# Optimization experiments

Measured on AMD Instinct MI355X. Metric: run time of the kernel, lower is better.

## Reference

```python
import jax, jax.numpy as jnp
import numpy as np

N, C, H, W = 4, 256, 128, 128
BLOCK = 8
FWB = H // BLOCK  # feature_size_with_block = 16
N_BBOX = 100
M = N_BBOX * N * FWB * FWB  # 102400 rois


def setup_inputs() -> dict:
    key = jax.random.key(0)
    ks = jax.random.split(key, 6)
    s = 1.0 / np.sqrt(C).astype(np.float32)
    return {
        "feature": jax.random.normal(ks[0], (N, C, H, W), jnp.float32),
        "rois_feature": jax.random.normal(ks[1], (M, C, 1, 1), jnp.float32),
        "W_weight": jax.random.normal(ks[2], (C, C), jnp.float32) * s,
        "b_weight": jnp.zeros((C,), jnp.float32),
        "W_fuse": jax.random.normal(ks[3], (C, C), jnp.float32) * s,
        "b_fuse": jnp.zeros((C,), jnp.float32),
        "W_pw": jax.random.normal(ks[4], (BLOCK * BLOCK, C), jnp.float32) * s,
        "b_pw": jnp.zeros((BLOCK * BLOCK,), jnp.float32),
        "feature_size_with_block": FWB,
    }


def reference(feature, rois_feature, W_weight, b_weight, W_fuse, b_fuse, W_pw, b_pw, feature_size_with_block):
    n, c, h, w = feature.shape
    f = feature_size_with_block
    blk = h // f  # block_size
    m = rois_feature.shape[0]
    n_bbox = m // (n * f * f)

    x = rois_feature[:, :, 0, 0]  # [M, C] (1x1 conv on 1x1 spatial == dense layer)
    feat_w = jax.nn.relu(x @ W_weight.T + b_weight)  # [M, C]
    feat_f = jax.nn.relu(x @ W_fuse.T + b_fuse)      # [M, C]
    point_weight = feat_w @ W_pw.T + b_pw            # [M, B*B]

    # [n_bbox, N, F, F, B, B] -> [N, n_bbox, F, F, B, B]
    pw = point_weight.reshape(n_bbox, n, f, f, blk, blk).transpose(1, 0, 2, 3, 4, 5)
    # feature -> blocks: [N, C, F, B, F, B] -> [N, C, F, F, B, B]
    fb = feature.reshape(n, c, f, blk, f, blk).transpose(0, 1, 2, 4, 3, 5)
    # weighted block-sum without materializing the n_bbox-repeated tensor.
    # torch: sum over (B,B) -> [N,nb,C,F,F], then permute(1,0,3,4,2) -> [nb,N,F,F,C]
    out = jnp.einsum('ncpqab,nkpqab->knpqc', fb, pw)  # [nb, N, F, F, C]
    out = out.reshape(m, c)[:, :, None, None]          # [M, C, 1, 1]
    fused = feat_f[:, :, None, None] + out
    return fused, out
```

## Files before the change

### kernel.cpp

```cpp
#include <hip/hip_runtime.h>

#define NN 4
#define CC 256
#define HH 128
#define FWBv 16
#define BLK 8
#define NBBOX 100
#define MM (NBBOX * NN * FWBv * FWBv)

typedef __attribute__((ext_vector_type(8))) short bf16x8;
typedef __attribute__((ext_vector_type(4))) float f32x4;

__device__ __forceinline__ unsigned short f2bf(float x) {
  union { float f; unsigned int u; } v; v.f = x;
  unsigned int r = v.u + 0x7FFFu + ((v.u >> 16) & 1u);
  return (unsigned short)(r >> 16);
}

__device__ __forceinline__ float bfbits2f(unsigned int hi16) {
  union { float f; unsigned int u; } v; v.u = hi16;
  return v.f;
}

__device__ __forceinline__ void async16(const void* g, void* l) {
  __builtin_amdgcn_global_load_lds(
      (__attribute__((address_space(1))) void*)(g),
      (__attribute__((address_space(3))) void*)(l), 16, 0, 0);
}

__global__ __launch_bounds__(256) void k_convert(
    const float* __restrict__ Wf, const float* __restrict__ Ww,
    const float* __restrict__ Wpw,
    unsigned short* __restrict__ oWf, unsigned short* __restrict__ oWw,
    unsigned short* __restrict__ oWpw) {
  int i = blockIdx.x * 256 + threadIdx.x;
  oWf[i] = f2bf(Wf[i]);
  oWw[i] = f2bf(Ww[i]);
  if (i < 64 * 256) oWpw[i] = f2bf(Wpw[i]);
}


__device__ __forceinline__ void stage_w(const unsigned short* __restrict__ Wp,
                                        int kc, unsigned short* buf, int w,
                                        int lane) {
  const int srcs = ((lane & 3) ^ ((lane >> 3) & 3)) * 8;
  const int rr = lane >> 2;
#pragma unroll
  for (int i = 0; i < 4; ++i) {
    const int r0 = w * 64 + i * 16;
    async16(Wp + (size_t)(r0 + rr) * 256 + kc * 32 + srcs, buf + r0 * 32);
  }
}

__device__ __forceinline__ void stage_wpw(const unsigned short* __restrict__ Wpw,
                                          unsigned short* buf, int kc4, int w,
                                          int lane) {
  const int srcs = ((lane & 7) ^ ((lane >> 3) & 7)) * 8;
  const int rr = lane >> 3;
#pragma unroll
  for (int i = 0; i < 2; ++i) {
    const int r0 = w * 16 + i * 8;
    async16(Wpw + (size_t)(r0 + rr) * 256 + kc4 * 64 + srcs, buf + r0 * 64);
  }
}

__device__ __forceinline__ void body16(const unsigned short* buf,
                                       const unsigned short (*xsp)[264],
                                       int kcol, int w, int lr, int quad,
                                       int wslot, f32x4 acc[4][4]) {
  bf16x8 aw[4], bx[4];
#pragma unroll
  for (int nt = 0; nt < 4; ++nt)
    aw[nt] = *(const bf16x8*)&buf[(w * 64 + nt * 16 + lr) * 32 + wslot];
#pragma unroll
  for (int mt = 0; mt < 4; ++mt)
    bx[mt] = *(const bf16x8*)&xsp[mt * 16 + lr][kcol];
  __builtin_amdgcn_s_setprio(1);
#pragma unroll
  for (int mt = 0; mt < 4; ++mt)
#pragma unroll
    for (int nt = 0; nt < 4; ++nt)
      acc[mt][nt] = __builtin_amdgcn_mfma_f32_16x16x32_bf16(
          aw[nt], bx[mt], acc[mt][nt], 0, 0, 0);
  __builtin_amdgcn_s_setprio(0);
}

__global__ __launch_bounds__(256) void k1(
    const float* __restrict__ rois,
    const unsigned short* __restrict__ Wf,
    const unsigned short* __restrict__ Ww,
    const unsigned short* __restrict__ Wpw,
    const float* __restrict__ bf_, const float* __restrict__ bw_,
    const float* __restrict__ bpw_,
    float* __restrict__ out_slot)
{
  __shared__ __align__(16) unsigned short xs[64][264];
  __shared__ __align__(16) unsigned short bs[2][8192];
  unsigned short* bsf = &bs[0][0];
  unsigned short* os = (unsigned short*)out_slot;
  const int t = threadIdx.x;
  const int lane = t & 63, w = t >> 6;
  const int lr = lane & 15, quad = lane >> 4;
  const int row_base = blockIdx.x * 64;
  const int wslot = (quad ^ ((lr >> 1) & 3)) << 3;

  stage_w(Wf, 0, &bs[0][0], w, lane);

#pragma unroll
  for (int i = 0; i < 16; ++i) {
    const int elem = (i * 256 + t) * 4;
    const int r = elem >> 8, c = elem & 255;
    const float4 v = *(const float4*)(rois + (size_t)row_base * 256 + elem);
    unsigned int lo = f2bf(v.x) | ((unsigned int)f2bf(v.y) << 16);
    unsigned int hi = f2bf(v.z) | ((unsigned int)f2bf(v.w) << 16);
    *(uint2*)&xs[r][c] = make_uint2(lo, hi);
  }
  asm volatile("s_waitcnt vmcnt(0) lgkmcnt(0)" ::: "memory");
  __builtin_amdgcn_s_barrier();

  f32x4 acc[4][4];
#pragma unroll
  for (int mt = 0; mt < 4; ++mt)
#pragma unroll
    for (int nt = 0; nt < 4; ++nt) acc[mt][nt] = (f32x4){0.f, 0.f, 0.f, 0.f};

#pragma unroll
  for (int kc = 0; kc < 8; ++kc) {
    if (kc < 7) stage_w(Wf, kc + 1, &bs[(kc + 1) & 1][0], w, lane);
    else        stage_w(Ww, 0, &bs[0][0], w, lane);
    asm volatile("s_waitcnt vmcnt(4)" ::: "memory");
    body16(&bs[kc & 1][0], xs, kc * 32 + quad * 8, w, lr, quad, wslot, acc);
  }

#pragma unroll
  for (int nt = 0; nt < 4; ++nt) {
    const int col0 = w * 64 + nt * 16 + quad * 4;
    const float4 b4 = *(const float4*)(bf_ + col0);
#pragma unroll
    for (int mt = 0; mt < 4; ++mt) {
      float v0 = acc[mt][nt][0] + b4.x; v0 = v0 > 0.f ? v0 : 0.f;
      float v1 = acc[mt][nt][1] + b4.y; v1 = v1 > 0.f ? v1 : 0.f;
      float v2 = acc[mt][nt][2] + b4.z; v2 = v2 > 0.f ? v2 : 0.f;
      float v3 = acc[mt][nt][3] + b4.w; v3 = v3 > 0.f ? v3 : 0.f;
      unsigned int lo = f2bf(v0) | ((unsigned int)f2bf(v1) << 16);
      unsigned int hi = f2bf(v2) | ((unsigned int)f2bf(v3) << 16);
      *(uint2*)&os[(size_t)(row_base + mt * 16 + lr) * 512 + 128 + col0] =
          make_uint2(lo, hi);
      acc[mt][nt] = (f32x4){0.f, 0.f, 0.f, 0.f};
    }
  }

#pragma unroll
  for (int kc = 0; kc < 8; ++kc) {
    if (kc < 7) {
      stage_w(Ww, kc + 1, &bs[(kc + 1) & 1][0], w, lane);
      asm volatile("s_waitcnt vmcnt(4)" ::: "memory");
    } else {
      asm volatile("s_waitcnt vmcnt(0)" ::: "memory");
    }
    body16(&bs[kc & 1][0], xs, kc * 32 + quad * 8, w, lr, quad, wslot, acc);
  }

  __builtin_amdgcn_s_barrier();

#pragma unroll
  for (int c = 0; c < 4; ++c) stage_wpw(Wpw, bsf + c * 4096, c, w, lane);

#pragma unroll
  for (int nt = 0; nt < 4; ++nt) {
    const int col0 = w * 64 + nt * 16 + quad * 4;
    const float4 b4 = *(const float4*)(bw_ + col0);
#pragma unroll
    for (int mt = 0; mt < 4; ++mt) {
      float v0 = acc[mt][nt][0] + b4.x; v0 = v0 > 0.f ? v0 : 0.f;
      float v1 = acc[mt][nt][1] + b4.y; v1 = v1 > 0.f ? v1 : 0.f;
      float v2 = acc[mt][nt][2] + b4.z; v2 = v2 > 0.f ? v2 : 0.f;
      float v3 = acc[mt][nt][3] + b4.w; v3 = v3 > 0.f ? v3 : 0.f;
      unsigned int lo = f2bf(v0) | ((unsigned int)f2bf(v1) << 16);
      unsigned int hi = f2bf(v2) | ((unsigned int)f2bf(v3) << 16);
      *(uint2*)&xs[mt * 16 + lr][col0] = make_uint2(lo, hi);
    }
  }
  asm volatile("s_waitcnt vmcnt(0) lgkmcnt(0)" ::: "memory");
  __builtin_amdgcn_s_barrier();

  f32x4 acc2[4];
#pragma unroll
  for (int mt = 0; mt < 4; ++mt) acc2[mt] = (f32x4){0.f, 0.f, 0.f, 0.f};
#pragma unroll
  for (int c = 0; c < 4; ++c) {
#pragma unroll
    for (int kt = 0; kt < 2; ++kt) {
      const int sl = ((kt * 4 + quad) ^ (lr & 7)) << 3;
      const bf16x8 apw =
          *(const bf16x8*)&bsf[c * 4096 + (w * 16 + lr) * 64 + sl];
      const int kcol = c * 64 + kt * 32 + quad * 8;
      __builtin_amdgcn_s_setprio(1);
#pragma unroll
      for (int mt = 0; mt < 4; ++mt) {
        const bf16x8 bx = *(const bf16x8*)&xs[mt * 16 + lr][kcol];
        acc2[mt] =
            __builtin_amdgcn_mfma_f32_16x16x32_bf16(apw, bx, acc2[mt], 0, 0, 0);
      }
      __builtin_amdgcn_s_setprio(0);
    }
  }
  {
    const int j0 = w * 16 + quad * 4;
    const float4 bj = *(const float4*)(bpw_ + j0);
#pragma unroll
    for (int mt = 0; mt < 4; ++mt) {
      float v0 = acc2[mt][0] + bj.x;
      float v1 = acc2[mt][1] + bj.y;
      float v2 = acc2[mt][2] + bj.z;
      float v3 = acc2[mt][3] + bj.w;
      unsigned int lo = f2bf(v0) | ((unsigned int)f2bf(v1) << 16);
      unsigned int hi = f2bf(v2) | ((unsigned int)f2bf(v3) << 16);
      *(uint2*)&os[(size_t)(row_base + mt * 16 + lr) * 512 + j0] =
          make_uint2(lo, hi);
    }
  }
}

__global__ __launch_bounds__(512) void k2(
    const float* __restrict__ feature,
    float* __restrict__ fused_slot,
    float* __restrict__ out_slot)
{
  __shared__ unsigned short fbuf[256][72];
  __shared__ unsigned short pwb[112][72];
  const int t = threadIdx.x;
  const int lane = t & 63, w = t >> 6;
  const int lr = lane & 15, quad = lane >> 4;
  const int bid = blockIdx.x;
  const int n = bid >> 8, p = (bid >> 4) & 15, q = bid & 15;
  const unsigned short* os = (const unsigned short*)out_slot;

  if (t < 432) {
    const int r = 100 + t / 36, cw = t % 36;
    *(unsigned int*)&pwb[r][cw * 2] = 0u;
  }

  for (int pi = t; pi < 2048; pi += 512) {
    const int c = pi >> 3, a = pi & 7;
    const float* fp =
        feature + (((size_t)n * 256 + c) * 128 + p * 8 + a) * 128 + q * 8;
    const float4 v0 = *(const float4*)fp;
    const float4 v1 = *(const float4*)(fp + 4);
    unsigned int u0 = f2bf(v0.x) | ((unsigned int)f2bf(v0.y) << 16);
    unsigned int u1 = f2bf(v0.z) | ((unsigned int)f2bf(v0.w) << 16);
    unsigned int u2 = f2bf(v1.x) | ((unsigned int)f2bf(v1.y) << 16);
    unsigned int u3 = f2bf(v1.z) | ((unsigned int)f2bf(v1.w) << 16);
    *(uint4*)&fbuf[c][a * 8] = make_uint4(u0, u1, u2, u3);
  }

  for (int pi = t; pi < 1600; pi += 512) {
    const int k = pi >> 4, ch = pi & 15;
    const uint2 v = *(const uint2*)&os[(size_t)(bid + k * 1024) * 512 + ch * 4];
    *(uint2*)&pwb[k][ch * 4] = v;
  }
  __syncthreads();

  uint2 ffp[7][2];
#pragma unroll
  for (int kt = 0; kt < 7; ++kt) {
    const int k = kt * 16 + lr;
    if (k < 100) {
      const size_t ro = (size_t)(bid + k * 1024) * 512;
#pragma unroll
      for (int ct = 0; ct < 2; ++ct) {
        const int c0 = w * 32 + ct * 16 + quad * 4;
        ffp[kt][ct] = *(const uint2*)&os[ro + 128 + c0];
      }
    }
  }

  f32x4 acc[7][2];
#pragma unroll
  for (int kt = 0; kt < 7; ++kt)
#pragma unroll
    for (int ct = 0; ct < 2; ++ct) acc[kt][ct] = (f32x4){0.f, 0.f, 0.f, 0.f};
#pragma unroll
  for (int kj = 0; kj < 2; ++kj) {
    const int kk = kj * 32 + quad * 8;
    bf16x8 pa[7], fa[2];
#pragma unroll
    for (int kt = 0; kt < 7; ++kt)
      pa[kt] = *(const bf16x8*)&pwb[kt * 16 + lr][kk];
#pragma unroll
    for (int ct = 0; ct < 2; ++ct)
      fa[ct] = *(const bf16x8*)&fbuf[w * 32 + ct * 16 + lr][kk];
    __builtin_amdgcn_s_setprio(1);
#pragma unroll
    for (int kt = 0; kt < 7; ++kt)
#pragma unroll
      for (int ct = 0; ct < 2; ++ct)
        acc[kt][ct] = __builtin_amdgcn_mfma_f32_16x16x32_bf16(
            fa[ct], pa[kt], acc[kt][ct], 0, 0, 0);
    __builtin_amdgcn_s_setprio(0);
  }

  asm volatile("s_waitcnt vmcnt(0)" ::: "memory");
  __builtin_amdgcn_s_barrier();

#pragma unroll
  for (int kt = 0; kt < 7; ++kt) {
    const int k = kt * 16 + lr;
    if (k < 100) {
      const size_t ro = (size_t)(bid + k * 1024) * 256;
#pragma unroll
      for (int ct = 0; ct < 2; ++ct) {
        const int c0 = w * 32 + ct * 16 + quad * 4;
        float4 v;
        v.x = acc[kt][ct][0];
        v.y = acc[kt][ct][1];
        v.z = acc[kt][ct][2];
        v.w = acc[kt][ct][3];
        *(float4*)(out_slot + ro + c0) = v;
        const uint2 ff = ffp[kt][ct];
        float4 f;
        f.x = v.x + bfbits2f(ff.x << 16);
        f.y = v.y + bfbits2f(ff.x & 0xffff0000u);
        f.z = v.z + bfbits2f(ff.y << 16);
        f.w = v.w + bfbits2f(ff.y & 0xffff0000u);
        *(float4*)(fused_slot + ro + c0) = f;
      }
    }
  }
}

extern "C" void kernel_launch(void* const* d_in, const int* in_sizes, int n_in,
                              void* d_out, int out_size, void* d_ws, size_t ws_size,
                              hipStream_t stream) {
  const float* feature = (const float*)d_in[0];
  const float* rois = (const float*)d_in[1];
  const float* Ww = (const float*)d_in[2];
  const float* bw = (const float*)d_in[3];
  const float* Wf = (const float*)d_in[4];
  const float* bfv = (const float*)d_in[5];
  const float* Wpw = (const float*)d_in[6];
  const float* bpw = (const float*)d_in[7];

  unsigned short* wsWf = (unsigned short*)d_ws;
  unsigned short* wsWw = wsWf + 256 * 256;
  unsigned short* wsWpw = wsWw + 256 * 256;

  float* fused_slot = (float*)d_out;
  float* out_slot = fused_slot + (size_t)MM * 256;

  k_convert<<<256, 256, 0, stream>>>(Wf, Ww, Wpw, wsWf, wsWw, wsWpw);
  k1<<<MM / 64, 256, 0, stream>>>(rois, wsWf, wsWw, wsWpw, bfv, bw, bpw,
                                  out_slot);
  k2<<<NN * FWBv * FWBv, 512, 0, stream>>>(feature, fused_slot, out_slot);
}
```

Before: 455.8 us.

## Pre-swizzle weights into MFMA fragment order and load them directly into registers

The weight conversion kernel now writes bf16 weights in a fragment-major layout that matches the MFMA A-operand, so k1 can load each fragment straight from global memory into registers. This replaces the async global-to-LDS staging buffers, their waitcnts and the swizzled LDS reads. LDS use drops, which allows a launch bound of 3 blocks per CU for more occupancy. The cost is more VGPRs for the double-buffered fragments and more global/L2 traffic, because every block now reads the weights directly rather than through shared staging.

Result: faster. 441.4 us (-3.1%).

```diff
diff --git a/kernel.cpp b/kernel.cpp
--- a/kernel.cpp
+++ b/kernel.cpp
@@ -22,10 +22,8 @@
   return v.f;
 }
 
-__device__ __forceinline__ void async16(const void* g, void* l) {
-  __builtin_amdgcn_global_load_lds(
-      (__attribute__((address_space(1))) void*)(g),
-      (__attribute__((address_space(3))) void*)(l), 16, 0, 0);
+__device__ __forceinline__ unsigned int pk(float a, float b) {
+  return (unsigned int)f2bf(a) | ((unsigned int)f2bf(b) << 16);
 }
 
 __global__ __launch_bounds__(256) void k_convert(
@@ -33,45 +31,44 @@
     const float* __restrict__ Wpw,
     unsigned short* __restrict__ oWf, unsigned short* __restrict__ oWw,
     unsigned short* __restrict__ oWpw) {
-  int i = blockIdx.x * 256 + threadIdx.x;
-  oWf[i] = f2bf(Wf[i]);
-  oWw[i] = f2bf(Ww[i]);
-  if (i < 64 * 256) oWpw[i] = f2bf(Wpw[i]);
-}
-
-
-__device__ __forceinline__ void stage_w(const unsigned short* __restrict__ Wp,
-                                        int kc, unsigned short* buf, int w,
-                                        int lane) {
-  const int srcs = ((lane & 3) ^ ((lane >> 3) & 3)) * 8;
-  const int rr = lane >> 2;
-#pragma unroll
-  for (int i = 0; i < 4; ++i) {
-    const int r0 = w * 64 + i * 16;
-    async16(Wp + (size_t)(r0 + rr) * 256 + kc * 32 + srcs, buf + r0 * 32);
-  }
-}
-
-__device__ __forceinline__ void stage_wpw(const unsigned short* __restrict__ Wpw,
-                                          unsigned short* buf, int kc4, int w,
-                                          int lane) {
-  const int srcs = ((lane & 7) ^ ((lane >> 3) & 7)) * 8;
-  const int rr = lane >> 3;
-#pragma unroll
-  for (int i = 0; i < 2; ++i) {
-    const int r0 = w * 16 + i * 8;
-    async16(Wpw + (size_t)(r0 + rr) * 256 + kc4 * 64 + srcs, buf + r0 * 64);
-  }
-}
-
-__device__ __forceinline__ void body16(const unsigned short* buf,
-                                       const unsigned short (*xsp)[264],
-                                       int kcol, int w, int lr, int quad,
-                                       int wslot, f32x4 acc[4][4]) {
-  bf16x8 aw[4], bx[4];
-#pragma unroll
-  for (int nt = 0; nt < 4; ++nt)
-    aw[nt] = *(const bf16x8*)&buf[(w * 64 + nt * 16 + lr) * 32 + wslot];
+  const int i = blockIdx.x * 256 + threadIdx.x;
+  if (i < 8192) {
+    const int lane = i & 63, g = (i >> 6) & 15, kc = i >> 10;
+    const int row = g * 16 + (lane & 15);
+    const int col0 = kc * 32 + (lane >> 4) * 8;
+    {
+      const float* s = Wf + (size_t)row * 256 + col0;
+      const float4 a = *(const float4*)s, b = *(const float4*)(s + 4);
+      *(uint4*)(oWf + (size_t)i * 8) =
+          make_uint4(pk(a.x, a.y), pk(a.z, a.w), pk(b.x, b.y), pk(b.z, b.w));
+    }
+    {
+      const float* s = Ww + (size_t)row * 256 + col0;
+      const float4 a = *(const float4*)s, b = *(const float4*)(s + 4);
+      *(uint4*)(oWw + (size_t)i * 8) =
+          make_uint4(pk(a.x, a.y), pk(a.z, a.w), pk(b.x, b.y), pk(b.z, b.w));
+    }
+  } else {
+    const int j = i - 8192;
+    const int lane = j & 63, g = (j >> 6) & 3, kc = j >> 8;
+    const int row = g * 16 + (lane & 15);
+    const int col0 = kc * 32 + (lane >> 4) * 8;
+    const float* s = Wpw + (size_t)row * 256 + col0;
+    const float4 a = *(const float4*)s, b = *(const float4*)(s + 4);
+    *(uint4*)(oWpw + (size_t)j * 8) =
+        make_uint4(pk(a.x, a.y), pk(a.z, a.w), pk(b.x, b.y), pk(b.z, b.w));
+  }
+}
+
+__device__ __forceinline__ bf16x8 ld_frag(const unsigned short* __restrict__ W,
+                                          int frag, int lane) {
+  return *(const bf16x8*)(W + (((size_t)frag * 64 + lane) << 3));
+}
+
+__device__ __forceinline__ void bodyR(const bf16x8 aw[4],
+                                      const unsigned short (*xsp)[264],
+                                      int kcol, int lr, f32x4 acc[4][4]) {
+  bf16x8 bx[4];
 #pragma unroll
   for (int mt = 0; mt < 4; ++mt)
     bx[mt] = *(const bf16x8*)&xsp[mt * 16 + lr][kcol];
@@ -85,7 +82,7 @@
   __builtin_amdgcn_s_setprio(0);
 }
 
-__global__ __launch_bounds__(256) void k1(
+__global__ __launch_bounds__(256, 3) void k1(
     const float* __restrict__ rois,
     const unsigned short* __restrict__ Wf,
     const unsigned short* __restrict__ Ww,
@@ -95,27 +92,25 @@
     float* __restrict__ out_slot)
 {
   __shared__ __align__(16) unsigned short xs[64][264];
-  __shared__ __align__(16) unsigned short bs[2][8192];
-  unsigned short* bsf = &bs[0][0];
   unsigned short* os = (unsigned short*)out_slot;
   const int t = threadIdx.x;
   const int lane = t & 63, w = t >> 6;
   const int lr = lane & 15, quad = lane >> 4;
   const int row_base = blockIdx.x * 64;
-  const int wslot = (quad ^ ((lr >> 1) & 3)) << 3;
-
-  stage_w(Wf, 0, &bs[0][0], w, lane);
+  const int w4 = w * 4;
+
+  bf16x8 aw[2][4];
+#pragma unroll
+  for (int nt = 0; nt < 4; ++nt) aw[0][nt] = ld_frag(Wf, w4 + nt, lane);
 
 #pragma unroll
   for (int i = 0; i < 16; ++i) {
     const int elem = (i * 256 + t) * 4;
     const int r = elem >> 8, c = elem & 255;
     const float4 v = *(const float4*)(rois + (size_t)row_base * 256 + elem);
-    unsigned int lo = f2bf(v.x) | ((unsigned int)f2bf(v.y) << 16);
-    unsigned int hi = f2bf(v.z) | ((unsigned int)f2bf(v.w) << 16);
-    *(uint2*)&xs[r][c] = make_uint2(lo, hi);
-  }
-  asm volatile("s_waitcnt vmcnt(0) lgkmcnt(0)" ::: "memory");
+    *(uint2*)&xs[r][c] = make_uint2(pk(v.x, v.y), pk(v.z, v.w));
+  }
+  asm volatile("s_waitcnt lgkmcnt(0)" ::: "memory");
   __builtin_amdgcn_s_barrier();
 
   f32x4 acc[4][4];
@@ -126,10 +121,12 @@
 
 #pragma unroll
   for (int kc = 0; kc < 8; ++kc) {
-    if (kc < 7) stage_w(Wf, kc + 1, &bs[(kc + 1) & 1][0], w, lane);
-    else        stage_w(Ww, 0, &bs[0][0], w, lane);
-    asm volatile("s_waitcnt vmcnt(4)" ::: "memory");
-    body16(&bs[kc & 1][0], xs, kc * 32 + quad * 8, w, lr, quad, wslot, acc);
+    const unsigned short* nsrc = (kc < 7) ? Wf : Ww;
+    const int nkc = (kc < 7) ? kc + 1 : 0;
+#pragma unroll
+    for (int nt = 0; nt < 4; ++nt)
+      aw[(kc + 1) & 1][nt] = ld_frag(nsrc, nkc * 16 + w4 + nt, lane);
+    bodyR(aw[kc & 1], xs, kc * 32 + quad * 8, lr, acc);
   }
 
 #pragma unroll
@@ -142,10 +139,8 @@
       float v1 = acc[mt][nt][1] + b4.y; v1 = v1 > 0.f ? v1 : 0.f;
       float v2 = acc[mt][nt][2] + b4.z; v2 = v2 > 0.f ? v2 : 0.f;
       float v3 = acc[mt][nt][3] + b4.w; v3 = v3 > 0.f ? v3 : 0.f;
-      unsigned int lo = f2bf(v0) | ((unsigned int)f2bf(v1) << 16);
-      unsigned int hi = f2bf(v2) | ((unsigned int)f2bf(v3) << 16);
       *(uint2*)&os[(size_t)(row_base + mt * 16 + lr) * 512 + 128 + col0] =
-          make_uint2(lo, hi);
+          make_uint2(pk(v0, v1), pk(v2, v3));
       acc[mt][nt] = (f32x4){0.f, 0.f, 0.f, 0.f};
     }
   }
@@ -153,18 +148,19 @@
 #pragma unroll
   for (int kc = 0; kc < 8; ++kc) {
     if (kc < 7) {
-      stage_w(Ww, kc + 1, &bs[(kc + 1) & 1][0], w, lane);
-      asm volatile("s_waitcnt vmcnt(4)" ::: "memory");
-    } else {
-      asm volatile("s_waitcnt vmcnt(0)" ::: "memory");
-    }
-    body16(&bs[kc & 1][0], xs, kc * 32 + quad * 8, w, lr, quad, wslot, acc);
-  }
+#pragma unroll
+      for (int nt = 0; nt < 4; ++nt)
+        aw[(kc + 1) & 1][nt] = ld_frag(Ww, (kc + 1) * 16 + w4 + nt, lane);
+    }
+    bodyR(aw[kc & 1], xs, kc * 32 + quad * 8, lr, acc);
+  }
+
+  bf16x8 apw[8];
+#pragma unroll
+  for (int idx = 0; idx < 8; ++idx)
+    apw[idx] = ld_frag(Wpw, idx * 4 + w, lane);
 
   __builtin_amdgcn_s_barrier();
-
-#pragma unroll
-  for (int c = 0; c < 4; ++c) stage_wpw(Wpw, bsf + c * 4096, c, w, lane);
 
 #pragma unroll
   for (int nt = 0; nt < 4; ++nt) {
@@ -176,48 +172,36 @@
       float v1 = acc[mt][nt][1] + b4.y; v1 = v1 > 0.f ? v1 : 0.f;
       float v2 = acc[mt][nt][2] + b4.z; v2 = v2 > 0.f ? v2 : 0.f;
       float v3 = acc[mt][nt][3] + b4.w; v3 = v3 > 0.f ? v3 : 0.f;
-      unsigned int lo = f2bf(v0) | ((unsigned int)f2bf(v1) << 16);
-      unsigned int hi = f2bf(v2) | ((unsigned int)f2bf(v3) << 16);
-      *(uint2*)&xs[mt * 16 + lr][col0] = make_uint2(lo, hi);
-    }
-  }
-  asm volatile("s_waitcnt vmcnt(0) lgkmcnt(0)" ::: "memory");
+      *(uint2*)&xs[mt * 16 + lr][col0] = make_uint2(pk(v0, v1), pk(v2, v3));
+    }
+  }
+  asm volatile("s_waitcnt lgkmcnt(0)" ::: "memory");
   __builtin_amdgcn_s_barrier();
 
   f32x4 acc2[4];
 #pragma unroll
   for (int mt = 0; mt < 4; ++mt) acc2[mt] = (f32x4){0.f, 0.f, 0.f, 0.f};
 #pragma unroll
-  for (int c = 0; c < 4; ++c) {
-#pragma unroll
-    for (int kt = 0; kt < 2; ++kt) {
-      const int sl = ((kt * 4 + quad) ^ (lr & 7)) << 3;
-      const bf16x8 apw =
-          *(const bf16x8*)&bsf[c * 4096 + (w * 16 + lr) * 64 + sl];
-      const int kcol = c * 64 + kt * 32 + quad * 8;
-      __builtin_amdgcn_s_setprio(1);
-#pragma unroll
-      for (int mt = 0; mt < 4; ++mt) {
-        const bf16x8 bx = *(const bf16x8*)&xs[mt * 16 + lr][kcol];
-        acc2[mt] =
-            __builtin_amdgcn_mfma_f32_16x16x32_bf16(apw, bx, acc2[mt], 0, 0, 0);
-      }
-      __builtin_amdgcn_s_setprio(0);
-    }
+  for (int idx = 0; idx < 8; ++idx) {
+    const int kcol = idx * 32 + quad * 8;
+    __builtin_amdgcn_s_setprio(1);
+#pragma unroll
+    for (int mt = 0; mt < 4; ++mt) {
+      const bf16x8 bx = *(const bf16x8*)&xs[mt * 16 + lr][kcol];
+      acc2[mt] =
+          __builtin_amdgcn_mfma_f32_16x16x32_bf16(apw[idx], bx, acc2[mt], 0, 0, 0);
+    }
+    __builtin_amdgcn_s_setprio(0);
   }
   {
     const int j0 = w * 16 + quad * 4;
     const float4 bj = *(const float4*)(bpw_ + j0);
 #pragma unroll
     for (int mt = 0; mt < 4; ++mt) {
-      float v0 = acc2[mt][0] + bj.x;
-      float v1 = acc2[mt][1] + bj.y;
-      float v2 = acc2[mt][2] + bj.z;
-      float v3 = acc2[mt][3] + bj.w;
-      unsigned int lo = f2bf(v0) | ((unsigned int)f2bf(v1) << 16);
-      unsigned int hi = f2bf(v2) | ((unsigned int)f2bf(v3) << 16);
+      const float v0 = acc2[mt][0] + bj.x, v1 = acc2[mt][1] + bj.y;
+      const float v2 = acc2[mt][2] + bj.z, v3 = acc2[mt][3] + bj.w;
       *(uint2*)&os[(size_t)(row_base + mt * 16 + lr) * 512 + j0] =
-          make_uint2(lo, hi);
+          make_uint2(pk(v0, v1), pk(v2, v3));
     }
   }
 }
@@ -247,11 +231,8 @@
         feature + (((size_t)n * 256 + c) * 128 + p * 8 + a) * 128 + q * 8;
     const float4 v0 = *(const float4*)fp;
     const float4 v1 = *(const float4*)(fp + 4);
-    unsigned int u0 = f2bf(v0.x) | ((unsigned int)f2bf(v0.y) << 16);
-    unsigned int u1 = f2bf(v0.z) | ((unsigned int)f2bf(v0.w) << 16);
-    unsigned int u2 = f2bf(v1.x) | ((unsigned int)f2bf(v1.y) << 16);
-    unsigned int u3 = f2bf(v1.z) | ((unsigned int)f2bf(v1.w) << 16);
-    *(uint4*)&fbuf[c][a * 8] = make_uint4(u0, u1, u2, u3);
+    *(uint4*)&fbuf[c][a * 8] =
+        make_uint4(pk(v0.x, v0.y), pk(v0.z, v0.w), pk(v1.x, v1.y), pk(v1.z, v1.w));
   }
 
   for (int pi = t; pi < 1600; pi += 512) {
@@ -348,7 +329,7 @@
   float* fused_slot = (float*)d_out;
   float* out_slot = fused_slot + (size_t)MM * 256;
 
-  k_convert<<<256, 256, 0, stream>>>(Wf, Ww, Wpw, wsWf, wsWw, wsWpw);
+  k_convert<<<40, 256, 0, stream>>>(Wf, Ww, Wpw, wsWf, wsWw, wsWpw);
   k1<<<MM / 64, 256, 0, stream>>>(rois, wsWf, wsWw, wsWpw, bfv, bw, bpw,
                                   out_slot);
   k2<<<NN * FWBv * FWBv, 512, 0, stream>>>(feature, fused_slot, out_slot);
```
